# Performance work log

Measured on AMD Instinct MI355X. Metric: run time of the kernel, lower is better.

Reference implementation:

```python
import jax, jax.numpy as jnp
import numpy as np

LAT_MIN, LAT_MAX = -90.0, 90.0
LON_MIN, LON_MAX = 0.0, 360.0
N_LEVELS = 4
N_FEAT = 2
FINEST = 0.25
BASE = 1.0
LAT_SHAPE, LON_SHAPE = 720, 1440
GEODESIC_WEIGHT = True
TABLE = (LAT_SHAPE + 1) * (LON_SHAPE + 1)  # 1038961
# corner offsets in the torch BOX_OFFSETS order: (0,0),(0,1),(1,0),(1,1)
OFFS = np.array([[0, 0], [0, 1], [1, 0], [1, 1]], dtype=np.int32)


def setup_inputs() -> dict:
    key = jax.random.key(0)
    k1, k2 = jax.random.split(key)
    B = 2_000_000
    u = jax.random.uniform(k1, (B, 2), dtype=jnp.float32)
    # lat in [-90, 90), lon in [0, 360)
    x = jnp.stack([u[:, 0] * 180.0 - 90.0, u[:, 1] * 360.0], axis=1)
    embeddings = jax.random.uniform(k2, (N_LEVELS, TABLE, N_FEAT),
                                    minval=-1e-4, maxval=1e-4, dtype=jnp.float32)
    return {"x": x, "embeddings": embeddings}


def _geodesic(lat1, lon1, lat2, lon2):
    r = jnp.pi / 180.0
    rl1, rl2 = lat1 * r, lat2 * r
    dlat = (lat2 - lat1) * r
    dlon = (lon2 - lon1) * r
    a = jnp.sin(dlat / 2) ** 2 + jnp.cos(rl1) * jnp.cos(rl2) * jnp.sin(dlon / 2) ** 2
    return 2.0 * jnp.arctan2(jnp.sqrt(a), jnp.sqrt(1.0 - a))


def reference(x, embeddings):
    box_min = jnp.array([LAT_MIN - FINEST, LON_MIN - FINEST], dtype=x.dtype)
    box_max = jnp.array([LAT_MAX + FINEST, LON_MAX + FINEST], dtype=x.dtype)
    xc = jnp.clip(x, box_min, box_max)  # clamped coords used for grid indexing
    offs = jnp.asarray(OFFS)
    outs = []
    for i in range(N_LEVELS):
        gs = BASE * (2.0 ** i)  # grid size (same for lat and lon)
        bl = jnp.floor((xc - box_min) / gs).astype(jnp.int32)  # [B,2] bottom-left idx
        gmin = bl.astype(x.dtype) * gs + box_min                # [B,2]
        gmax = gmin + gs
        width = int(np.floor(LON_SHAPE / gs))
        # 4 corner flat indices: lat_idx * width + lon_idx -> [B,4]
        idx = (bl[:, 0:1] + offs[None, :, 0]) * width + (bl[:, 1:2] + offs[None, :, 1])
        e = embeddings[i][idx]  # gather: [B,4,F]
        if GEODESIC_WEIGHT:
            wlat = _geodesic(gmin[:, 0], gmin[:, 1], x[:, 0], gmin[:, 1]) / \
                   _geodesic(gmin[:, 0], gmin[:, 1], gmax[:, 0], gmin[:, 1])
            wlon = _geodesic(gmin[:, 0], x[:, 1], gmin[:, 0], gmax[:, 1]) / \
                   _geodesic(gmin[:, 0], gmin[:, 1], gmin[:, 0], gmax[:, 1])
        else:
            w = (x - gmin) / (gmax - gmin)
            wlat, wlon = w[:, 0], w[:, 1]
        # bilinear blend (corner order: 0=(0,0) 1=(0,1) 2=(1,0) 3=(1,1))
        c0 = e[:, 0] * (1 - wlat[:, None]) + e[:, 2] * wlat[:, None]
        c1 = e[:, 1] * (1 - wlat[:, None]) + e[:, 3] * wlat[:, None]
        outs.append(c0 * (1 - wlon[:, None]) + c1 * wlon[:, None])
    return jnp.concatenate(outs, axis=-1)  # [B, N_LEVELS*N_FEAT]
```

## Files before the change

### kernel.cpp

```cpp
#include <hip/hip_runtime.h>
#include <hip/hip_fp16.h>

#define NT 256
#define PPT 4

constexpr int TABLE_SZ = 721 * 1441;

constexpr int QLAT = 181, QLON = 361;
constexpr int NCELLS = QLAT * QLON;

constexpr int LUT_OFF0 = 0, LUT_OFF1 = 181, LUT_OFF2 = 272, LUT_OFF3 = 318;
constexpr int LUT_N = 341;

typedef float v4f __attribute__((ext_vector_type(4)));
typedef float v2f __attribute__((ext_vector_type(2)));

__device__ __constant__ float c_s2_tab[4] = {0.008726535498f, 0.017452406437f,
                                             0.034899496703f, 0.069756473744f};

__global__ __launch_bounds__(256)
void build_superquad(const float* __restrict__ emb, uint4* __restrict__ sq)
{
    int c = blockIdx.x * 256 + threadIdx.x;
    if (c >= NCELLS) return;
    int la = c / QLON, lo = c - la * QLON;
    const float2* embv = (const float2*)emb;
    #pragma unroll
    for (int i = 0; i < 4; ++i) {
        const int width = 1440 >> i;
        const int ra = la >> i, co = lo >> i;
        const float2* t = embv + (size_t)i * TABLE_SZ;
        float2 e0 = t[ra * width + co];
        float2 e1 = t[ra * width + co + 1];
        float2 e2 = t[(ra + 1) * width + co];
        float2 e3 = t[(ra + 1) * width + co + 1];
        union { uint4 u; __half2 h[4]; } pk;
        pk.h[0] = __floats2half2_rn(e0.x, e0.y);
        pk.h[1] = __floats2half2_rn(e1.x, e1.y);
        pk.h[2] = __floats2half2_rn(e2.x, e2.y);
        pk.h[3] = __floats2half2_rn(e3.x, e3.y);
        sq[(size_t)c * 4 + i] = pk.u;
    }
}

__global__ __launch_bounds__(NT)
void ngp_interp_mp(const float* __restrict__ x,
                   const uint4* __restrict__ sq,
                   float* __restrict__ out,
                   int B)
{
    const float r = 0.017453292519943295f;
    const float bmin_lat = -90.25f;
    const float bmin_lon = -0.25f;
    const float bmax_lat = 90.25f, bmax_lon = 360.25f;

    const int t = threadIdx.x;
    const int base = blockIdx.x * (NT * PPT) + t;

    int pidx[PPT];
    v2f xp[PPT];
    #pragma unroll
    for (int k = 0; k < PPT; ++k) {
        const int p = base + k * NT;
        pidx[k] = p;
        const int pc = p < B ? p : B - 1;
        xp[k] = __builtin_nontemporal_load(reinterpret_cast<const v2f*>(x) + pc);
    }

    __shared__ float2 lut[LUT_N];
    for (int i = t; i < LUT_N; i += NT) {
        int lvl, row;
        if (i < LUT_OFF1)      { lvl = 0; row = i; }
        else if (i < LUT_OFF2) { lvl = 1; row = i - LUT_OFF1; }
        else if (i < LUT_OFF3) { lvl = 2; row = i - LUT_OFF2; }
        else                   { lvl = 3; row = i - LUT_OFF3; }
        const float gs = (float)(1 << lvl);
        const float gmin_lat = (float)row * gs + bmin_lat;
        const float ca = fabsf(__cosf(gmin_lat * r));
        const float z2 = ca * c_s2_tab[lvl];
        const float n2 = z2 + z2 * z2 * z2 * (1.0f / 6.0f);
        lut[i] = make_float2(ca, __builtin_amdgcn_rcpf(n2));
    }
    __syncthreads();

    float vlat[PPT], vlon[PPT];
    uint4 g[PPT][4];
    #pragma unroll
    for (int k = 0; k < PPT; ++k) {
        const float xlat = xp[k].x;
        const float xlon = xp[k].y;
        const float xc_lat = fminf(fmaxf(xlat, bmin_lat), bmax_lat);
        const float xc_lon = fminf(fmaxf(xlon, bmin_lon), bmax_lon);
        vlat[k] = xc_lat - bmin_lat;
        vlon[k] = xc_lon - bmin_lon;
        const int cell0 = (int)floorf(vlat[k]) * QLON + (int)floorf(vlon[k]);
        const uint4* cellp = sq + (size_t)cell0 * 4;
        g[k][0] = cellp[0];
        g[k][1] = cellp[1];
        g[k][2] = cellp[2];
        g[k][3] = cellp[3];
    }

    const int lut_off[4] = {LUT_OFF0, LUT_OFF1, LUT_OFF2, LUT_OFF3};

    #pragma unroll
    for (int k = 0; k < PPT; ++k) {
        const float xlat = xp[k].x;
        const float xlon = xp[k].y;
        const float v_lat = vlat[k];
        const float v_lon = vlon[k];

        float o[8];
        #pragma unroll
        for (int i = 0; i < 4; ++i) {
            const float gs     = (float)(1 << i);
            const float inv_gs = 1.0f / gs;

            const float blat_f = floorf(v_lat * inv_gs);
            const float blon_f = floorf(v_lon * inv_gs);
            const float gmin_lat = blat_f * gs + bmin_lat;
            const float gmin_lon = blon_f * gs + bmin_lon;
            const float gmax_lon = gmin_lon + gs;
            const int bl_lat = (int)blat_f;

            union { uint4 u; __half2 h[4]; } pk;
            pk.u = g[k][i];
            const float2 f0 = __half22float2(pk.h[0]);
            const float2 f1 = __half22float2(pk.h[1]);
            const float2 f2 = __half22float2(pk.h[2]);
            const float2 f3 = __half22float2(pk.h[3]);
            const v2f E0 = {f0.x, f0.y}, E1 = {f1.x, f1.y};
            const v2f E2 = {f2.x, f2.y}, E3 = {f3.x, f3.y};

            const float wlat = (xlat - gmin_lat) * inv_gs;

            const float2 cl = lut[lut_off[i] + bl_lat];
            const float h1 = (gmax_lon - xlon) * r * 0.5f;
            const float s1 = h1 - h1 * h1 * h1 * (1.0f / 6.0f);
            const float z1 = cl.x * s1;
            const float n1 = z1 + z1 * z1 * z1 * (1.0f / 6.0f);
            const float wlon = n1 * cl.y;

            const v2f wa = {wlat, wlat};
            const v2f wo = {wlon, wlon};
            const v2f c0 = E0 + (E2 - E0) * wa;
            const v2f c1 = E1 + (E3 - E1) * wa;
            const v2f res = c0 + (c1 - c0) * wo;
            o[2*i]   = res.x;
            o[2*i+1] = res.y;
        }

        if (pidx[k] < B) {
            v4f* op = reinterpret_cast<v4f*>(out + (size_t)pidx[k] * 8);
            const v4f lo = {o[0], o[1], o[2], o[3]};
            const v4f hi = {o[4], o[5], o[6], o[7]};
            __builtin_nontemporal_store(lo, op);
            __builtin_nontemporal_store(hi, op + 1);
        }
    }
}

__global__ __launch_bounds__(NT)
void ngp_interp_fb(const float* __restrict__ x,
                   const float* __restrict__ emb,
                   float* __restrict__ out,
                   int B)
{
    const float r = 0.017453292519943295f;
    const float bmin_lat = -90.25f;
    const float bmin_lon = -0.25f;

    __shared__ float2 lut[LUT_N];
    for (int t = threadIdx.x; t < LUT_N; t += NT) {
        int lvl, row;
        if (t < LUT_OFF1)      { lvl = 0; row = t; }
        else if (t < LUT_OFF2) { lvl = 1; row = t - LUT_OFF1; }
        else if (t < LUT_OFF3) { lvl = 2; row = t - LUT_OFF2; }
        else                   { lvl = 3; row = t - LUT_OFF3; }
        const float gs = (float)(1 << lvl);
        const float gmin_lat = (float)row * gs + bmin_lat;
        const float ca = fabsf(__cosf(gmin_lat * r));
        const float z2 = ca * c_s2_tab[lvl];
        const float n2 = z2 + z2 * z2 * z2 * (1.0f / 6.0f);
        lut[t] = make_float2(ca, __builtin_amdgcn_rcpf(n2));
    }
    __syncthreads();

    const int p = blockIdx.x * NT + threadIdx.x;
    if (p >= B) return;

    const v2f xp = __builtin_nontemporal_load(reinterpret_cast<const v2f*>(x) + p);
    const float xlat = xp.x;
    const float xlon = xp.y;

    const float bmax_lat = 90.25f, bmax_lon = 360.25f;
    const float xc_lat = fminf(fmaxf(xlat, bmin_lat), bmax_lat);
    const float xc_lon = fminf(fmaxf(xlon, bmin_lon), bmax_lon);
    const float v_lat = xc_lat - bmin_lat;
    const float v_lon = xc_lon - bmin_lon;

    const int lut_off[4] = {LUT_OFF0, LUT_OFF1, LUT_OFF2, LUT_OFF3};
    float o[8];

    #pragma unroll
    for (int i = 0; i < 4; ++i) {
        const float gs     = (float)(1 << i);
        const float inv_gs = 1.0f / gs;
        const int   width  = 1440 >> i;

        const float blat_f = floorf(v_lat * inv_gs);
        const float blon_f = floorf(v_lon * inv_gs);
        const float gmin_lat = blat_f * gs + bmin_lat;
        const float gmin_lon = blon_f * gs + bmin_lon;
        const float gmax_lon = gmin_lon + gs;
        const int bl_lat = (int)blat_f;
        const int bl_lon = (int)blon_f;

        const int idx00 = bl_lat * width + bl_lon;
        const float* base0 = emb + ((size_t)i * TABLE_SZ + (size_t)idx00) * 2;
        const float* base1 = base0 + (size_t)width * 2;
        v4f eA, eB;
        __builtin_memcpy(&eA, base0, 16);
        __builtin_memcpy(&eB, base1, 16);
        const v2f E0 = {eA.x, eA.y}, E1 = {eA.z, eA.w};
        const v2f E2 = {eB.x, eB.y}, E3 = {eB.z, eB.w};

        const float wlat = (xlat - gmin_lat) * inv_gs;

        const float2 cl = lut[lut_off[i] + bl_lat];
        const float h1 = (gmax_lon - xlon) * r * 0.5f;
        const float s1 = h1 - h1 * h1 * h1 * (1.0f / 6.0f);
        const float z1 = cl.x * s1;
        const float n1 = z1 + z1 * z1 * z1 * (1.0f / 6.0f);
        const float wlon = n1 * cl.y;

        const v2f wa = {wlat, wlat};
        const v2f wo = {wlon, wlon};
        const v2f c0 = E0 + (E2 - E0) * wa;
        const v2f c1 = E1 + (E3 - E1) * wa;
        const v2f res = c0 + (c1 - c0) * wo;
        o[2*i]   = res.x;
        o[2*i+1] = res.y;
    }

    v4f* op = reinterpret_cast<v4f*>(out + (size_t)p * 8);
    const v4f lo = {o[0], o[1], o[2], o[3]};
    const v4f hi = {o[4], o[5], o[6], o[7]};
    __builtin_nontemporal_store(lo, op);
    __builtin_nontemporal_store(hi, op + 1);
}

extern "C" void kernel_launch(void* const* d_in, const int* in_sizes, int n_in,
                              void* d_out, int out_size, void* d_ws, size_t ws_size,
                              hipStream_t stream)
{
    const float* x   = (const float*)d_in[0];
    const float* emb = (const float*)d_in[1];
    float* out = (float*)d_out;
    const int B = in_sizes[0] / 2;

    const size_t sq_bytes = (size_t)NCELLS * 64;
    if (ws_size >= sq_bytes) {
        uint4* sq = (uint4*)d_ws;
        build_superquad<<<(NCELLS + 255) / 256, 256, 0, stream>>>(emb, sq);
        const int pts_per_blk = NT * PPT;
        const int grid = (B + pts_per_blk - 1) / pts_per_blk;
        ngp_interp_mp<<<grid, NT, 0, stream>>>(x, sq, out, B);
    } else {
        const int grid = (B + NT - 1) / NT;
        ngp_interp_fb<<<grid, NT, 0, stream>>>(x, emb, out, B);
    }
}
```

Measured before the change: 120.2 us.

## Split interpolation across four lanes per point, one lane per level

Each point is now handled by four adjacent threads, with each thread taking one resolution level. Each lane loads one 16-byte superquad entry and writes one 8-byte output slice, so gathers and stores across a group are contiguous 64- and 32-byte accesses. The goal is more memory-level parallelism and coalescing, and fewer registers per thread. In exchange, each lane redundantly loads the point coordinates, which quadruples reads of x, and it launches four times as many blocks.

```diff
diff --git a/kernel.cpp b/kernel.cpp
--- a/kernel.cpp
+++ b/kernel.cpp
@@ -44,7 +44,7 @@
 }
 
 __global__ __launch_bounds__(NT)
-void ngp_interp_mp(const float* __restrict__ x,
+void ngp_interp_lv(const float* __restrict__ x,
                    const uint4* __restrict__ sq,
                    float* __restrict__ out,
                    int B)
@@ -54,14 +54,21 @@
     const float bmin_lon = -0.25f;
     const float bmax_lat = 90.25f, bmax_lon = 360.25f;
 
-    const int t = threadIdx.x;
-    const int base = blockIdx.x * (NT * PPT) + t;
+    const int t   = threadIdx.x;
+    const int lvl = t & 3;
+    const int pg  = t >> 2;
+    const int pbase = blockIdx.x * ((NT / 4) * PPT) + pg;
+
+    const float gs     = __int_as_float(0x3f800000 + (lvl << 23));
+    const float inv_gs = __int_as_float(0x3f800000 - (lvl << 23));
+    const int lut_off_l = (lvl >= 1 ? 181 : 0) + (lvl >= 2 ? 91 : 0)
+                        + (lvl >= 3 ? 46 : 0);
 
     int pidx[PPT];
     v2f xp[PPT];
     #pragma unroll
     for (int k = 0; k < PPT; ++k) {
-        const int p = base + k * NT;
+        const int p = pbase + k * (NT / 4);
         pidx[k] = p;
         const int pc = p < B ? p : B - 1;
         xp[k] = __builtin_nontemporal_load(reinterpret_cast<const v2f*>(x) + pc);
@@ -69,22 +76,22 @@
 
     __shared__ float2 lut[LUT_N];
     for (int i = t; i < LUT_N; i += NT) {
-        int lvl, row;
-        if (i < LUT_OFF1)      { lvl = 0; row = i; }
-        else if (i < LUT_OFF2) { lvl = 1; row = i - LUT_OFF1; }
-        else if (i < LUT_OFF3) { lvl = 2; row = i - LUT_OFF2; }
-        else                   { lvl = 3; row = i - LUT_OFF3; }
-        const float gs = (float)(1 << lvl);
-        const float gmin_lat = (float)row * gs + bmin_lat;
+        int lv, row;
+        if (i < LUT_OFF1)      { lv = 0; row = i; }
+        else if (i < LUT_OFF2) { lv = 1; row = i - LUT_OFF1; }
+        else if (i < LUT_OFF3) { lv = 2; row = i - LUT_OFF2; }
+        else                   { lv = 3; row = i - LUT_OFF3; }
+        const float gsl = (float)(1 << lv);
+        const float gmin_lat = (float)row * gsl + bmin_lat;
         const float ca = fabsf(__cosf(gmin_lat * r));
-        const float z2 = ca * c_s2_tab[lvl];
+        const float z2 = ca * c_s2_tab[lv];
         const float n2 = z2 + z2 * z2 * z2 * (1.0f / 6.0f);
         lut[i] = make_float2(ca, __builtin_amdgcn_rcpf(n2));
     }
     __syncthreads();
 
     float vlat[PPT], vlon[PPT];
-    uint4 g[PPT][4];
+    uint4 g[PPT];
     #pragma unroll
     for (int k = 0; k < PPT; ++k) {
         const float xlat = xp[k].x;
@@ -94,14 +101,8 @@
         vlat[k] = xc_lat - bmin_lat;
         vlon[k] = xc_lon - bmin_lon;
         const int cell0 = (int)floorf(vlat[k]) * QLON + (int)floorf(vlon[k]);
-        const uint4* cellp = sq + (size_t)cell0 * 4;
-        g[k][0] = cellp[0];
-        g[k][1] = cellp[1];
-        g[k][2] = cellp[2];
-        g[k][3] = cellp[3];
-    }
-
-    const int lut_off[4] = {LUT_OFF0, LUT_OFF1, LUT_OFF2, LUT_OFF3};
+        g[k] = sq[(size_t)cell0 * 4 + lvl];
+    }
 
     #pragma unroll
     for (int k = 0; k < PPT; ++k) {
@@ -110,52 +111,40 @@
         const float v_lat = vlat[k];
         const float v_lon = vlon[k];
 
-        float o[8];
-        #pragma unroll
-        for (int i = 0; i < 4; ++i) {
-            const float gs     = (float)(1 << i);
-            const float inv_gs = 1.0f / gs;
-
-            const float blat_f = floorf(v_lat * inv_gs);
-            const float blon_f = floorf(v_lon * inv_gs);
-            const float gmin_lat = blat_f * gs + bmin_lat;
-            const float gmin_lon = blon_f * gs + bmin_lon;
-            const float gmax_lon = gmin_lon + gs;
-            const int bl_lat = (int)blat_f;
-
-            union { uint4 u; __half2 h[4]; } pk;
-            pk.u = g[k][i];
-            const float2 f0 = __half22float2(pk.h[0]);
-            const float2 f1 = __half22float2(pk.h[1]);
-            const float2 f2 = __half22float2(pk.h[2]);
-            const float2 f3 = __half22float2(pk.h[3]);
-            const v2f E0 = {f0.x, f0.y}, E1 = {f1.x, f1.y};
-            const v2f E2 = {f2.x, f2.y}, E3 = {f3.x, f3.y};
-
-            const float wlat = (xlat - gmin_lat) * inv_gs;
-
-            const float2 cl = lut[lut_off[i] + bl_lat];
-            const float h1 = (gmax_lon - xlon) * r * 0.5f;
-            const float s1 = h1 - h1 * h1 * h1 * (1.0f / 6.0f);
-            const float z1 = cl.x * s1;
-            const float n1 = z1 + z1 * z1 * z1 * (1.0f / 6.0f);
-            const float wlon = n1 * cl.y;
-
-            const v2f wa = {wlat, wlat};
-            const v2f wo = {wlon, wlon};
-            const v2f c0 = E0 + (E2 - E0) * wa;
-            const v2f c1 = E1 + (E3 - E1) * wa;
-            const v2f res = c0 + (c1 - c0) * wo;
-            o[2*i]   = res.x;
-            o[2*i+1] = res.y;
-        }
+        const float blat_f = floorf(v_lat * inv_gs);
+        const float blon_f = floorf(v_lon * inv_gs);
+        const float gmin_lat = blat_f * gs + bmin_lat;
+        const float gmin_lon = blon_f * gs + bmin_lon;
+        const float gmax_lon = gmin_lon + gs;
+        const int bl_lat = (int)blat_f;
+
+        union { uint4 u; __half2 h[4]; } pk;
+        pk.u = g[k];
+        const float2 f0 = __half22float2(pk.h[0]);
+        const float2 f1 = __half22float2(pk.h[1]);
+        const float2 f2 = __half22float2(pk.h[2]);
+        const float2 f3 = __half22float2(pk.h[3]);
+        const v2f E0 = {f0.x, f0.y}, E1 = {f1.x, f1.y};
+        const v2f E2 = {f2.x, f2.y}, E3 = {f3.x, f3.y};
+
+        const float wlat = (xlat - gmin_lat) * inv_gs;
+
+        const float2 cl = lut[lut_off_l + bl_lat];
+        const float h1 = (gmax_lon - xlon) * r * 0.5f;
+        const float s1 = h1 - h1 * h1 * h1 * (1.0f / 6.0f);
+        const float z1 = cl.x * s1;
+        const float n1 = z1 + z1 * z1 * z1 * (1.0f / 6.0f);
+        const float wlon = n1 * cl.y;
+
+        const v2f wa = {wlat, wlat};
+        const v2f wo = {wlon, wlon};
+        const v2f c0 = E0 + (E2 - E0) * wa;
+        const v2f c1 = E1 + (E3 - E1) * wa;
+        const v2f res = c0 + (c1 - c0) * wo;
 
         if (pidx[k] < B) {
-            v4f* op = reinterpret_cast<v4f*>(out + (size_t)pidx[k] * 8);
-            const v4f lo = {o[0], o[1], o[2], o[3]};
-            const v4f hi = {o[4], o[5], o[6], o[7]};
-            __builtin_nontemporal_store(lo, op);
-            __builtin_nontemporal_store(hi, op + 1);
+            v2f* op = reinterpret_cast<v2f*>(out + (size_t)pidx[k] * 8 + lvl * 2);
+            __builtin_nontemporal_store(res, op);
         }
     }
 }
@@ -263,9 +252,9 @@
     if (ws_size >= sq_bytes) {
         uint4* sq = (uint4*)d_ws;
         build_superquad<<<(NCELLS + 255) / 256, 256, 0, stream>>>(emb, sq);
-        const int pts_per_blk = NT * PPT;
+        const int pts_per_blk = (NT / 4) * PPT;
         const int grid = (B + pts_per_blk - 1) / pts_per_blk;
-        ngp_interp_mp<<<grid, NT, 0, stream>>>(x, sq, out, B);
+        ngp_interp_lv<<<grid, NT, 0, stream>>>(x, sq, out, B);
     } else {
         const int grid = (B + NT - 1) / NT;
         ngp_interp_fb<<<grid, NT, 0, stream>>>(x, emb, out, B);
```

Result: no change. 120.7 us (+0.4%).
